# Kernel optimization log

Hardware: AMD Instinct MI355X
Metric: run time of the kernel (lower is better)

The kernel has to match this reference:

```python
import math
import jax, jax.numpy as jnp
import numpy as np

D_MODEL = 512
MAX_SEQ = 512
NUM_OUT = 16
H = 1  # num_heads


def _pos_encoding(d_model, seq_len):
    # sinusoidal PE, then flipped along the sequence axis (ReversedPositionalEncoding)
    pos = jnp.arange(seq_len, dtype=jnp.float32)[:, None]
    i = jnp.arange(0, d_model, 2, dtype=jnp.float32)
    ang = pos * jnp.exp(i * (-(math.log(10000.0) / d_model)))  # [S, d/2]
    pe = jnp.stack([jnp.sin(ang), jnp.cos(ang)], axis=-1).reshape(seq_len, d_model)
    return pe[::-1]


def _layernorm(x, w, b, eps=1e-5):
    m = jnp.mean(x, axis=-1, keepdims=True)
    v = jnp.mean(jnp.square(x - m), axis=-1, keepdims=True)
    return (x - m) / jnp.sqrt(v + eps) * w + b


def setup_inputs() -> dict:
    key = jax.random.key(0)
    ks = jax.random.split(key, 8)
    B = 128
    latents = jax.random.normal(ks[0], (B, D_MODEL, MAX_SEQ), dtype=jnp.float32)
    query_mask = jnp.ones((B, NUM_OUT), dtype=jnp.float32)
    query = 0.02 * jax.random.normal(ks[1], (NUM_OUT, D_MODEL), dtype=jnp.float32)
    return {
        "latents": latents,
        "query_mask": query_mask,
        "query": query,
        "ln_lat_w": jnp.ones((D_MODEL,), jnp.float32),
        "ln_lat_b": jnp.zeros((D_MODEL,), jnp.float32),
        "ln_q_w": jnp.ones((D_MODEL,), jnp.float32),
        "ln_q_b": jnp.zeros((D_MODEL,), jnp.float32),
        "Wq": 0.02 * jax.random.normal(ks[2], (D_MODEL, D_MODEL), jnp.float32),
        "bq": jnp.zeros((D_MODEL,), jnp.float32),
        "Wk": 0.02 * jax.random.normal(ks[3], (D_MODEL, D_MODEL), jnp.float32),
        "bk": jnp.zeros((D_MODEL,), jnp.float32),
        "Wv": 0.02 * jax.random.normal(ks[4], (D_MODEL, D_MODEL), jnp.float32),
        "bv": jnp.zeros((D_MODEL,), jnp.float32),
        "Wo": 0.02 * jax.random.normal(ks[5], (1, D_MODEL), jnp.float32),
        "bo": jnp.zeros((1,), jnp.float32),
    }


def reference(latents, query_mask, query, ln_lat_w, ln_lat_b, ln_q_w, ln_q_b,
              Wq, bq, Wk, bk, Wv, bv, Wo, bo):
    B, _, N = latents.shape  # latents: [B, d_model, N]
    scale = math.sqrt(D_MODEL)
    Dh = D_MODEL // H

    # cross-attention mask: query_mask [B,Nq] x all-ones latent mask [B,N]
    mask = jnp.einsum('bq,bk->bqk', query_mask, jnp.ones((B, N), latents.dtype))

    x = jnp.swapaxes(latents, 1, 2) * scale           # [B, N, d]
    x = x + _pos_encoding(D_MODEL, MAX_SEQ)[-N:]      # reversed PE, last N positions
    # dropout is identity in eval mode
    x = _layernorm(x, ln_lat_w, ln_lat_b)

    q = _layernorm(query * scale, ln_q_w, ln_q_b)     # [Nq, d]
    q = jnp.broadcast_to(q[None], (B, NUM_OUT, D_MODEL))

    qh = (q @ Wq.T + bq).reshape(B, NUM_OUT, H, Dh)
    kh = (x @ Wk.T + bk).reshape(B, N, H, Dh)
    vh = (x @ Wv.T + bv).reshape(B, N, H, Dh)

    scores = jnp.einsum('bqhd,bkhd->bhqk', qh, kh) / math.sqrt(Dh)
    scores = jnp.where(mask[:, None] == 0, -1e9, scores)
    attn_weights = jax.nn.softmax(scores, axis=-1)    # [B, H, Nq, N]

    attn = jnp.einsum('bhqk,bkhd->bqhd', attn_weights, vh).reshape(B, NUM_OUT, H * Dh)
    wipe = jnp.all(mask == 0, axis=2, keepdims=True)  # [B, Nq, 1]
    attn = jnp.where(wipe, 0.0, attn)

    logits = attn @ Wo.T + bo                         # [B, Nq, 1]
    return logits, attn_weights
```

## Files before the change

kernel.cpp:

```cpp
#include <hip/hip_runtime.h>
#include <math.h>

#define DM 512
#define NQ 16
#define NG (NQ + 1)
#define NR (NG + 2)

typedef __attribute__((ext_vector_type(2))) float f32x2;
typedef __attribute__((ext_vector_type(4))) float f32x4;

__device__ __forceinline__ float wave_reduce_sum(float v) {
    #pragma unroll
    for (int off = 32; off > 0; off >>= 1) v += __shfl_xor(v, off, 64);
    return v;
}
__device__ __forceinline__ float wave_reduce_max(float v) {
    #pragma unroll
    for (int off = 32; off > 0; off >>= 1) v = fmaxf(v, __shfl_xor(v, off, 64));
    return v;
}

__global__ void k1_setup(const float* __restrict__ Wk, const float* __restrict__ Wv,
                         const float* __restrict__ query,
                         const float* __restrict__ ln_q_w, const float* __restrict__ ln_q_b,
                         const float* __restrict__ Wq, const float* __restrict__ bq,
                         float* __restrict__ PET, float* __restrict__ WkT,
                         float* __restrict__ WvT, float* __restrict__ qh, int N) {
    __shared__ float tile[64][65];
    int bx = blockIdx.x;
    int lane = threadIdx.x & 63;
    int w = threadIdx.x >> 6;

    if (bx < 128) {
        int ntile = bx & 7, jg = bx >> 3;
        int n = ntile * 64 + lane;
        float p = (float)(N - 1 - n);
        const float c = -logf(10000.f) / (float)DM;
        int jbase = jg * 16 + w * 4;
        #pragma unroll
        for (int u = 0; u < 4; ++u) {
            int j = jbase + u;
            float wj = expf((float)(2 * j) * c);
            float ang = p * wj;
            PET[(size_t)(2 * j) * N + n] = sinf(ang);
            PET[(size_t)(2 * j + 1) * N + n] = cosf(ang);
        }
    } else if (bx < 256) {
        int t = bx - 128;
        const float* W = (t >> 6) ? Wv : Wk;
        float* WT = (t >> 6) ? WvT : WkT;
        int tl = t & 63;
        int te = tl >> 3, td = tl & 7;
        #pragma unroll
        for (int i = 0; i < 16; ++i) {
            int el = w * 16 + i;
            tile[el][lane] = W[(size_t)(te * 64 + el) * DM + td * 64 + lane];
        }
        __syncthreads();
        #pragma unroll
        for (int i = 0; i < 16; ++i) {
            int dl = w * 16 + i;
            WT[(size_t)(td * 64 + dl) * DM + te * 64 + lane] = tile[lane][dl];
        }
    } else {
        int idx = (bx - 256) * 4 + w;
        int q = idx >> 9, e = idx & 511;
        const float scale = 22.627416997969522f;
        const float4* qr = (const float4*)(query + (size_t)q * DM);
        float4 a0 = qr[lane * 2], a1 = qr[lane * 2 + 1];
        a0.x *= scale; a0.y *= scale; a0.z *= scale; a0.w *= scale;
        a1.x *= scale; a1.y *= scale; a1.z *= scale; a1.w *= scale;
        float s  = a0.x + a0.y + a0.z + a0.w + a1.x + a1.y + a1.z + a1.w;
        float s2 = a0.x * a0.x + a0.y * a0.y + a0.z * a0.z + a0.w * a0.w
                 + a1.x * a1.x + a1.y * a1.y + a1.z * a1.z + a1.w * a1.w;
        s = wave_reduce_sum(s); s2 = wave_reduce_sum(s2);
        float m = s * (1.f / DM);
        float var = s2 * (1.f / DM) - m * m;
        float rstd = rsqrtf(var + 1e-5f);
        const float4* gw = (const float4*)ln_q_w;
        const float4* gb = (const float4*)ln_q_b;
        const float4* wr = (const float4*)(Wq + (size_t)e * DM);
        float4 w0 = gw[lane * 2], w1 = gw[lane * 2 + 1];
        float4 b0 = gb[lane * 2], b1 = gb[lane * 2 + 1];
        float4 W0 = wr[lane * 2], W1 = wr[lane * 2 + 1];
        float acc = ((a0.x - m) * rstd * w0.x + b0.x) * W0.x
                  + ((a0.y - m) * rstd * w0.y + b0.y) * W0.y
                  + ((a0.z - m) * rstd * w0.z + b0.z) * W0.z
                  + ((a0.w - m) * rstd * w0.w + b0.w) * W0.w
                  + ((a1.x - m) * rstd * w1.x + b1.x) * W1.x
                  + ((a1.y - m) * rstd * w1.y + b1.y) * W1.y
                  + ((a1.z - m) * rstd * w1.z + b1.z) * W1.z
                  + ((a1.w - m) * rstd * w1.w + b1.w) * W1.w;
        acc = wave_reduce_sum(acc);
        if (lane == 0) qh[q * DM + e] = acc + bq[e];
    }
}

__global__ void k3_qt(const float* __restrict__ qh, const float* __restrict__ WkT,
                      const float* __restrict__ Wo, const float* __restrict__ WvT,
                      const float* __restrict__ lnw,
                      float* __restrict__ qt, float* __restrict__ A,
                      f32x2* __restrict__ A2, float* __restrict__ wvout) {
    int idx = blockIdx.x * 4 + (threadIdx.x >> 6);
    int lane = threadIdx.x & 63;
    int g = idx >> 9, d = idx & 511;
    const float4* wr;
    const float4* xr;
    if (g < NQ) {
        wr = (const float4*)(WkT + (size_t)d * DM);
        xr = (const float4*)(qh + (size_t)g * DM);
    } else {
        wr = (const float4*)(WvT + (size_t)d * DM);
        xr = (const float4*)Wo;
    }
    float4 w0 = wr[lane * 2], w1 = wr[lane * 2 + 1];
    float4 x0 = xr[lane * 2], x1 = xr[lane * 2 + 1];
    float s = w0.x * x0.x + w0.y * x0.y + w0.z * x0.z + w0.w * x0.w
            + w1.x * x1.x + w1.y * x1.y + w1.z * x1.z + w1.w * x1.w;
    s = wave_reduce_sum(s);
    if (lane == 0) {
        if (g < NQ) qt[g * DM + d] = s;
        else wvout[d] = s;
        float a = s * lnw[d];
        A[g * DM + d] = a;
        f32x2 ap; ap.x = a; ap.y = a;
        A2[g * DM + d] = ap;
    }
}

__launch_bounds__(512, 4)
__global__ void main2_kernel(const float* __restrict__ latents,
                             const float* __restrict__ PET,
                             const f32x2* __restrict__ A2,
                             const float* __restrict__ A,
                             const float* __restrict__ qt,
                             const float* __restrict__ qh,
                             const float* __restrict__ wv,
                             const float* __restrict__ lnb,
                             const float* __restrict__ bk,
                             const float* __restrict__ Wo,
                             const float* __restrict__ bv,
                             float* __restrict__ pbuf,
                             float* __restrict__ consts, int N) {
    int B = gridDim.y - 1;
    int lane = threadIdx.x & 63;
    int w = threadIdx.x >> 6;
    int b = blockIdx.y;

    if (b == B) {
        int t = blockIdx.x * 8 + w;
        if (t > NQ) return;
        if (t < NQ) {
            float sa = 0.f, sc = 0.f, qb = 0.f;
            #pragma unroll
            for (int i = 0; i < 8; ++i) {
                int d = i * 64 + lane;
                sa += A[t * DM + d];
                sc = fmaf(qt[t * DM + d], lnb[d], sc);
                qb = fmaf(qh[t * DM + d], bk[d], qb);
            }
            sa = wave_reduce_sum(sa);
            sc = wave_reduce_sum(sc);
            qb = wave_reduce_sum(qb);
            if (lane == 0) { consts[t] = sa; consts[16 + t] = sc + qb; }
        } else {
            float sa = 0.f, cv = 0.f, bvo = 0.f;
            #pragma unroll
            for (int i = 0; i < 8; ++i) {
                int d = i * 64 + lane;
                sa += A[NQ * DM + d];
                cv = fmaf(wv[d], lnb[d], cv);
                bvo = fmaf(Wo[d], bv[d], bvo);
            }
            sa = wave_reduce_sum(sa);
            cv = wave_reduce_sum(cv);
            bvo = wave_reduce_sum(bvo);
            if (lane == 0) { consts[32] = sa; consts[33] = cv + bvo; }
        }
        return;
    }

    int ntile = blockIdx.x;
    int n0 = ntile * 128 + lane * 2;

    int d0 = __builtin_amdgcn_readfirstlane(w * 64);
    const float* latf = latents + (size_t)b * DM * N + (size_t)d0 * N + n0;
    const float* petf = PET + (size_t)d0 * N + n0;
    const float scale = 22.627416997969522f;
    f32x2 sc2; sc2.x = scale; sc2.y = scale;

    f32x2 acc[NG];
    #pragma unroll
    for (int i = 0; i < NG; ++i) { acc[i].x = 0.f; acc[i].y = 0.f; }
    f32x2 S1 = {0.f, 0.f}, S2 = {0.f, 0.f};

    const int U = 4;
    const int NC = 64 / U;
    f32x2 xb[2][U], pb[2][U];
    #pragma unroll
    for (int u = 0; u < U; ++u) {
        xb[0][u] = __builtin_nontemporal_load((const f32x2*)(latf + (size_t)u * N));
        pb[0][u] = *(const f32x2*)(petf + (size_t)u * N);
    }
    for (int c = 0; c < NC; c += 2) {
        #pragma unroll
        for (int u = 0; u < U; ++u) {
            size_t dd = (size_t)((c + 1) * U + u) * N;
            xb[1][u] = __builtin_nontemporal_load((const f32x2*)(latf + dd));
            pb[1][u] = *(const f32x2*)(petf + dd);
        }
        #pragma unroll
        for (int u = 0; u < U; ++u) {
            f32x2 y = xb[0][u] * sc2 + pb[0][u];
            S1 += y; S2 += y * y;
            int d = d0 + c * U + u;
            #pragma unroll
            for (int q = 0; q < NG; ++q)
                acc[q] += A2[(size_t)q * DM + d] * y;
        }
        if (c + 2 < NC) {
            #pragma unroll
            for (int u = 0; u < U; ++u) {
                size_t dd = (size_t)((c + 2) * U + u) * N;
                xb[0][u] = __builtin_nontemporal_load((const f32x2*)(latf + dd));
                pb[0][u] = *(const f32x2*)(petf + dd);
            }
        }
        #pragma unroll
        for (int u = 0; u < U; ++u) {
            f32x2 y = xb[1][u] * sc2 + pb[1][u];
            S1 += y; S2 += y * y;
            int d = d0 + (c + 1) * U + u;
            #pragma unroll
            for (int q = 0; q < NG; ++q)
                acc[q] += A2[(size_t)q * DM + d] * y;
        }
    }

    __shared__ f32x2 red[4][NR][64];
    if (w >= 4) {
        int ww = w - 4;
        red[ww][0][lane] = S1;
        red[ww][1][lane] = S2;
        #pragma unroll
        for (int i = 0; i < NG; ++i) red[ww][2 + i][lane] = acc[i];
    }
    __syncthreads();
    if (w < 4) {
        red[w][0][lane] += S1;
        red[w][1][lane] += S2;
        #pragma unroll
        for (int i = 0; i < NG; ++i) red[w][2 + i][lane] += acc[i];
    }
    __syncthreads();
    if (w == 0) {
        float* pout = pbuf + ((size_t)b * NR) * N + n0;
        #pragma unroll
        for (int i = 0; i < NR; ++i) {
            f32x2 t = red[0][i][lane] + red[1][i][lane]
                    + red[2][i][lane] + red[3][i][lane];
            *(f32x2*)(pout + (size_t)i * N) = t;
        }
    }
}

__global__ void k_fin(const float* __restrict__ pbuf,
                      const float* __restrict__ consts,
                      const float* __restrict__ query_mask,
                      const float* __restrict__ bo,
                      float* __restrict__ out_logits,
                      float* __restrict__ out_attn, int N, int B) {
    __shared__ float scs[NQ][512];
    __shared__ float vls[512];
    int b = blockIdx.x;
    int tid = threadIdx.x;
    const float isd = 0.044194173824159216f;
    float c32 = consts[32], c33 = consts[33];

    for (int np = tid; np < (N >> 1); np += 256) {
        int n0 = np * 2;
        const float* p = pbuf + ((size_t)b * NR) * N + n0;
        f32x2 tot[NR];
        #pragma unroll
        for (int i = 0; i < NR; ++i) tot[i] = *(const f32x2*)(p + (size_t)i * N);
        f32x2 m = tot[0] * (1.f / DM);
        f32x2 ex2 = tot[1] * (1.f / DM);
        f32x2 rstd;
        rstd.x = rsqrtf(ex2.x - m.x * m.x + 1e-5f);
        rstd.y = rsqrtf(ex2.y - m.y * m.y + 1e-5f);
        f32x2 v = rstd * (tot[2 + NQ] - m * c32) + c33;
        *(f32x2*)&vls[n0] = v;
        #pragma unroll
        for (int q = 0; q < NQ; ++q) {
            f32x2 sc = (rstd * (tot[2 + q] - m * consts[q]) + consts[16 + q]) * isd;
            *(f32x2*)&scs[q][n0] = sc;
        }
    }
    __syncthreads();

    int lane = tid & 63, w = tid >> 6;
    int nv = N >> 2;
    for (int q = w; q < NQ; q += 4) {
        int r = b * NQ + q;
        float qm = query_mask[r];
        f32x4* arow = (f32x4*)(out_attn + (size_t)r * N);
        if (qm == 0.f) {
            float u = 1.f / (float)N;
            f32x4 uv; uv.x = u; uv.y = u; uv.z = u; uv.w = u;
            for (int i = lane; i < nv; i += 64)
                __builtin_nontemporal_store(uv, &arow[i]);
            if (lane == 0) out_logits[r] = bo[0];
            continue;
        }
        const f32x4* srow = (const f32x4*)scs[q];
        f32x4 sv[2];
        sv[0] = srow[lane]; sv[1] = srow[64 + lane];
        float mx = fmaxf(fmaxf(fmaxf(sv[0].x, sv[0].y), fmaxf(sv[0].z, sv[0].w)),
                         fmaxf(fmaxf(sv[1].x, sv[1].y), fmaxf(sv[1].z, sv[1].w)));
        mx = wave_reduce_max(mx);
        float sum = 0.f;
        #pragma unroll
        for (int i = 0; i < 2; ++i) {
            sv[i].x = expf(sv[i].x - mx); sv[i].y = expf(sv[i].y - mx);
            sv[i].z = expf(sv[i].z - mx); sv[i].w = expf(sv[i].w - mx);
            sum += sv[i].x + sv[i].y + sv[i].z + sv[i].w;
        }
        sum = wave_reduce_sum(sum);
        float inv = 1.f / sum;
        const f32x4* vrow = (const f32x4*)vls;
        float lp = 0.f;
        #pragma unroll
        for (int i = 0; i < 2; ++i) {
            f32x4 vv = vrow[i * 64 + lane];
            f32x4 wgt = sv[i] * inv;
            __builtin_nontemporal_store(wgt, &arow[i * 64 + lane]);
            lp += wgt.x * vv.x + wgt.y * vv.y + wgt.z * vv.z + wgt.w * vv.w;
        }
        lp = wave_reduce_sum(lp);
        if (lane == 0) out_logits[r] = lp + bo[0];
    }
}

extern "C" void kernel_launch(void* const* d_in, const int* in_sizes, int n_in,
                              void* d_out, int out_size, void* d_ws, size_t ws_size,
                              hipStream_t stream) {
    const float* latents    = (const float*)d_in[0];
    const float* query_mask = (const float*)d_in[1];
    const float* query      = (const float*)d_in[2];
    const float* ln_lat_w   = (const float*)d_in[3];
    const float* ln_lat_b   = (const float*)d_in[4];
    const float* ln_q_w     = (const float*)d_in[5];
    const float* ln_q_b     = (const float*)d_in[6];
    const float* Wq         = (const float*)d_in[7];
    const float* bq         = (const float*)d_in[8];
    const float* Wk         = (const float*)d_in[9];
    const float* bk         = (const float*)d_in[10];
    const float* Wv         = (const float*)d_in[11];
    const float* bv         = (const float*)d_in[12];
    const float* Wo         = (const float*)d_in[13];
    const float* bo         = (const float*)d_in[14];

    int B = in_sizes[1] / NQ;
    int N = in_sizes[0] / (DM * B);

    float* ws = (float*)d_ws;
    size_t off = 0;
    float* PET    = ws + off; off += (size_t)DM * N;
    float* WkT    = ws + off; off += (size_t)DM * DM;
    float* WvT    = ws + off; off += (size_t)DM * DM;
    float* qh     = ws + off; off += NQ * DM;
    float* qt     = ws + off; off += NQ * DM;
    float* A      = ws + off; off += NG * DM;
    float* A2     = ws + off; off += (size_t)NG * DM * 2;
    float* wv     = ws + off; off += DM;
    float* consts = ws + off; off += 64;
    float* pbuf   = ws + off; off += (size_t)B * NR * N;

    float* out_logits = (float*)d_out;
    float* out_attn   = out_logits + (size_t)B * NQ;

    k1_setup<<<256 + NQ * DM / 4, 256, 0, stream>>>(
        Wk, Wv, query, ln_q_w, ln_q_b, Wq, bq, PET, WkT, WvT, qh, N);
    k3_qt<<<NG * DM / 4, 256, 0, stream>>>(qh, WkT, Wo, WvT, ln_lat_w,
                                           qt, A, (f32x2*)A2, wv);
    dim3 gmain(N >> 7, B + 1);
    main2_kernel<<<gmain, 512, 0, stream>>>(latents, PET, (const f32x2*)A2,
                                            A, qt, qh, wv, ln_lat_b, bk, Wo, bv,
                                            pbuf, consts, N);
    k_fin<<<B, 256, 0, stream>>>(pbuf, consts, query_mask, bo,
                                 out_logits, out_attn, N, B);
}
```

Baseline: 240.0 us.

## Fuse finalize into main kernel via last-block counter and atomic constant reduction

Removes the separate k_fin launch by having the last of the four column-tile blocks per batch (tracked with an atomic counter) perform the normalization, softmax and logits inside the main kernel. The per-query constants are now accumulated with atomicAdd in k3_qt, so the extra reduction block row and the A/qt/wv buffers go away. This saves one launch plus a pipeline drain, but concentrates the finalize work on a quarter of the blocks. The hardcoded count of 3 assumes N is 512, and the atomic float sums make the result order-dependent.

Measured after the change: 508.7 us. 2.12x slower.

```diff
diff --git a/kernel.cpp b/kernel.cpp
--- a/kernel.cpp
+++ b/kernel.cpp
@@ -25,13 +25,20 @@
                          const float* __restrict__ ln_q_w, const float* __restrict__ ln_q_b,
                          const float* __restrict__ Wq, const float* __restrict__ bq,
                          float* __restrict__ PET, float* __restrict__ WkT,
-                         float* __restrict__ WvT, float* __restrict__ qh, int N) {
+                         float* __restrict__ WvT, float* __restrict__ qh,
+                         float* __restrict__ consts, int* __restrict__ cnt,
+                         int N, int B) {
     __shared__ float tile[64][65];
     int bx = blockIdx.x;
     int lane = threadIdx.x & 63;
     int w = threadIdx.x >> 6;
 
     if (bx < 128) {
+        if (bx == 0) {
+            int tid = threadIdx.x;
+            if (tid < 34) consts[tid] = 0.f;
+            for (int i = tid; i < B; i += 256) cnt[i] = 0;
+        }
         int ntile = bx & 7, jg = bx >> 3;
         int n = ntile * 64 + lane;
         float p = (float)(N - 1 - n);
@@ -98,9 +105,9 @@
 
 __global__ void k3_qt(const float* __restrict__ qh, const float* __restrict__ WkT,
                       const float* __restrict__ Wo, const float* __restrict__ WvT,
-                      const float* __restrict__ lnw,
-                      float* __restrict__ qt, float* __restrict__ A,
-                      f32x2* __restrict__ A2, float* __restrict__ wvout) {
+                      const float* __restrict__ lnw, const float* __restrict__ lnb,
+                      const float* __restrict__ bk, const float* __restrict__ bv,
+                      f32x2* __restrict__ A2, float* __restrict__ consts) {
     int idx = blockIdx.x * 4 + (threadIdx.x >> 6);
     int lane = threadIdx.x & 63;
     int g = idx >> 9, d = idx & 511;
@@ -119,67 +126,33 @@
             + w1.x * x1.x + w1.y * x1.y + w1.z * x1.z + w1.w * x1.w;
     s = wave_reduce_sum(s);
     if (lane == 0) {
-        if (g < NQ) qt[g * DM + d] = s;
-        else wvout[d] = s;
         float a = s * lnw[d];
-        A[g * DM + d] = a;
         f32x2 ap; ap.x = a; ap.y = a;
-        A2[g * DM + d] = ap;
+        A2[(size_t)g * DM + d] = ap;
+        if (g < NQ) {
+            atomicAdd(&consts[g], a);
+            atomicAdd(&consts[16 + g], s * lnb[d] + qh[(size_t)g * DM + d] * bk[d]);
+        } else {
+            atomicAdd(&consts[32], a);
+            atomicAdd(&consts[33], s * lnb[d] + Wo[d] * bv[d]);
+        }
     }
 }
 
 __launch_bounds__(512, 4)
-__global__ void main2_kernel(const float* __restrict__ latents,
-                             const float* __restrict__ PET,
-                             const f32x2* __restrict__ A2,
-                             const float* __restrict__ A,
-                             const float* __restrict__ qt,
-                             const float* __restrict__ qh,
-                             const float* __restrict__ wv,
-                             const float* __restrict__ lnb,
-                             const float* __restrict__ bk,
-                             const float* __restrict__ Wo,
-                             const float* __restrict__ bv,
-                             float* __restrict__ pbuf,
-                             float* __restrict__ consts, int N) {
-    int B = gridDim.y - 1;
+__global__ void main_fused(const float* __restrict__ latents,
+                           const float* __restrict__ PET,
+                           const f32x2* __restrict__ A2,
+                           float* __restrict__ pbuf,
+                           int* __restrict__ cnt,
+                           const float* __restrict__ consts,
+                           const float* __restrict__ query_mask,
+                           const float* __restrict__ bo,
+                           float* __restrict__ out_logits,
+                           float* __restrict__ out_attn, int N) {
     int lane = threadIdx.x & 63;
     int w = threadIdx.x >> 6;
     int b = blockIdx.y;
-
-    if (b == B) {
-        int t = blockIdx.x * 8 + w;
-        if (t > NQ) return;
-        if (t < NQ) {
-            float sa = 0.f, sc = 0.f, qb = 0.f;
-            #pragma unroll
-            for (int i = 0; i < 8; ++i) {
-                int d = i * 64 + lane;
-                sa += A[t * DM + d];
-                sc = fmaf(qt[t * DM + d], lnb[d], sc);
-                qb = fmaf(qh[t * DM + d], bk[d], qb);
-            }
-            sa = wave_reduce_sum(sa);
-            sc = wave_reduce_sum(sc);
-            qb = wave_reduce_sum(qb);
-            if (lane == 0) { consts[t] = sa; consts[16 + t] = sc + qb; }
-        } else {
-            float sa = 0.f, cv = 0.f, bvo = 0.f;
-            #pragma unroll
-            for (int i = 0; i < 8; ++i) {
-                int d = i * 64 + lane;
-                sa += A[NQ * DM + d];
-                cv = fmaf(wv[d], lnb[d], cv);
-                bvo = fmaf(Wo[d], bv[d], bvo);
-            }
-            sa = wave_reduce_sum(sa);
-            cv = wave_reduce_sum(cv);
-            bvo = wave_reduce_sum(bvo);
-            if (lane == 0) { consts[32] = sa; consts[33] = cv + bvo; }
-        }
-        return;
-    }
-
     int ntile = blockIdx.x;
     int n0 = ntile * 128 + lane * 2;
 
@@ -237,7 +210,10 @@
         }
     }
 
-    __shared__ f32x2 red[4][NR][64];
+    __shared__ __align__(16) char smem[4 * NR * 64 * sizeof(f32x2)];
+    __shared__ int finflag;
+    f32x2 (*red)[NR][64] = (f32x2 (*)[NR][64])smem;
+
     if (w >= 4) {
         int ww = w - 4;
         red[ww][0][lane] = S1;
@@ -262,24 +238,23 @@
             *(f32x2*)(pout + (size_t)i * N) = t;
         }
     }
-}
-
-__global__ void k_fin(const float* __restrict__ pbuf,
-                      const float* __restrict__ consts,
-                      const float* __restrict__ query_mask,
-                      const float* __restrict__ bo,
-                      float* __restrict__ out_logits,
-                      float* __restrict__ out_attn, int N, int B) {
-    __shared__ float scs[NQ][512];
-    __shared__ float vls[512];
-    int b = blockIdx.x;
+
+    __threadfence();
+    __syncthreads();
+    if (threadIdx.x == 0) finflag = atomicAdd(&cnt[b], 1);
+    __syncthreads();
+    if (finflag != 3) return;
+    __threadfence();
+
+    float* scs = (float*)smem;
+    float* vls = (float*)(smem + NQ * 512 * sizeof(float));
     int tid = threadIdx.x;
     const float isd = 0.044194173824159216f;
     float c32 = consts[32], c33 = consts[33];
 
-    for (int np = tid; np < (N >> 1); np += 256) {
-        int n0 = np * 2;
-        const float* p = pbuf + ((size_t)b * NR) * N + n0;
+    for (int np = tid; np < (N >> 1); np += 512) {
+        int nn = np * 2;
+        const float* p = pbuf + ((size_t)b * NR) * N + nn;
         f32x2 tot[NR];
         #pragma unroll
         for (int i = 0; i < NR; ++i) tot[i] = *(const f32x2*)(p + (size_t)i * N);
@@ -289,18 +264,17 @@
         rstd.x = rsqrtf(ex2.x - m.x * m.x + 1e-5f);
         rstd.y = rsqrtf(ex2.y - m.y * m.y + 1e-5f);
         f32x2 v = rstd * (tot[2 + NQ] - m * c32) + c33;
-        *(f32x2*)&vls[n0] = v;
+        *(f32x2*)&vls[nn] = v;
         #pragma unroll
         for (int q = 0; q < NQ; ++q) {
             f32x2 sc = (rstd * (tot[2 + q] - m * consts[q]) + consts[16 + q]) * isd;
-            *(f32x2*)&scs[q][n0] = sc;
-        }
-    }
-    __syncthreads();
-
-    int lane = tid & 63, w = tid >> 6;
+            *(f32x2*)&scs[q * 512 + nn] = sc;
+        }
+    }
+    __syncthreads();
+
     int nv = N >> 2;
-    for (int q = w; q < NQ; q += 4) {
+    for (int q = w; q < NQ; q += 8) {
         int r = b * NQ + q;
         float qm = query_mask[r];
         f32x4* arow = (f32x4*)(out_attn + (size_t)r * N);
@@ -312,7 +286,7 @@
             if (lane == 0) out_logits[r] = bo[0];
             continue;
         }
-        const f32x4* srow = (const f32x4*)scs[q];
+        const f32x4* srow = (const f32x4*)(scs + q * 512);
         f32x4 sv[2];
         sv[0] = srow[lane]; sv[1] = srow[64 + lane];
         float mx = fmaxf(fmaxf(fmaxf(sv[0].x, sv[0].y), fmaxf(sv[0].z, sv[0].w)),
@@ -369,24 +343,21 @@
     float* WkT    = ws + off; off += (size_t)DM * DM;
     float* WvT    = ws + off; off += (size_t)DM * DM;
     float* qh     = ws + off; off += NQ * DM;
-    float* qt     = ws + off; off += NQ * DM;
-    float* A      = ws + off; off += NG * DM;
     float* A2     = ws + off; off += (size_t)NG * DM * 2;
-    float* wv     = ws + off; off += DM;
     float* consts = ws + off; off += 64;
+    int*   cnt    = (int*)(ws + off); off += 128;
     float* pbuf   = ws + off; off += (size_t)B * NR * N;
 
     float* out_logits = (float*)d_out;
     float* out_attn   = out_logits + (size_t)B * NQ;
 
     k1_setup<<<256 + NQ * DM / 4, 256, 0, stream>>>(
-        Wk, Wv, query, ln_q_w, ln_q_b, Wq, bq, PET, WkT, WvT, qh, N);
-    k3_qt<<<NG * DM / 4, 256, 0, stream>>>(qh, WkT, Wo, WvT, ln_lat_w,
-                                           qt, A, (f32x2*)A2, wv);
-    dim3 gmain(N >> 7, B + 1);
-    main2_kernel<<<gmain, 512, 0, stream>>>(latents, PET, (const f32x2*)A2,
-                                            A, qt, qh, wv, ln_lat_b, bk, Wo, bv,
-                                            pbuf, consts, N);
-    k_fin<<<B, 256, 0, stream>>>(pbuf, consts, query_mask, bo,
-                                 out_logits, out_attn, N, B);
-}
+        Wk, Wv, query, ln_q_w, ln_q_b, Wq, bq, PET, WkT, WvT, qh,
+        consts, cnt, N, B);
+    k3_qt<<<NG * DM / 4, 256, 0, stream>>>(qh, WkT, Wo, WvT, ln_lat_w, ln_lat_b,
+                                           bk, bv, (f32x2*)A2, consts);
+    dim3 gmain(N >> 7, B);
+    main_fused<<<gmain, 512, 0, stream>>>(latents, PET, (const f32x2*)A2,
+                                          pbuf, cnt, consts, query_mask, bo,
+                                          out_logits, out_attn, N);
+}
```
